# Performance work log

Hardware: AMD Instinct MI355X
Metric: run time of the kernel (lower is better)

Reference implementation:

```python
import jax, jax.numpy as jnp
import numpy as np

N, E, C, MID = 20000, 320000, 16, 32
EPS = 1e-8

# ---- real Clebsch-Gordan (Q_J) matrices for degree pairs up to l=1, real-SH m-order (-l..l) i.e. (y,z,x) for l=1 ----

def _q_matrices():
    Q0 = np.eye(3, dtype=np.float32)[:, :, None] / np.sqrt(3.0)          # 1x1 -> J=0
    eps = np.zeros((3, 3, 3), dtype=np.float32)
    for (a, b, c_) in [(0, 1, 2), (1, 2, 0), (2, 0, 1)]:
        eps[a, b, c_] = 1.0
        eps[a, c_, b] = -1.0
    Q1 = eps / np.sqrt(2.0)                                               # 1x1 -> J=1 (cross product)
    Q2 = np.zeros((3, 3, 5), dtype=np.float32)                            # 1x1 -> J=2 (sym traceless)
    s2 = 1.0 / np.sqrt(2.0); s6 = 1.0 / np.sqrt(6.0)
    Q2[2, 0, 0] = Q2[0, 2, 0] = s2          # ~xy
    Q2[0, 1, 1] = Q2[1, 0, 1] = s2          # ~yz
    Q2[0, 0, 2] = -s6; Q2[1, 1, 2] = 2 * s6; Q2[2, 2, 2] = -s6  # ~(2z2-x2-y2)
    Q2[1, 2, 3] = Q2[2, 1, 3] = s2          # ~xz
    Q2[2, 2, 4] = s2; Q2[0, 0, 4] = -s2     # ~(x2-y2)
    return Q0, Q1, Q2

_Q0, _Q1, _Q2 = _q_matrices()


def _basis(u):
    """u: [E,3] unit edge directions -> basis tensors per (d_in,d_out) pair."""
    x, y, z = u[:, 0], u[:, 1], u[:, 2]
    Ep = u.shape[0]
    Y0 = jnp.full((Ep,), 0.28209479177387814, u.dtype)
    Y1 = 0.4886025119029199 * jnp.stack([y, z, x], -1)                    # m=-1,0,1
    Y2 = jnp.stack([1.0925484305920792 * x * y,
                    1.0925484305920792 * y * z,
                    0.31539156525252005 * (3.0 * z * z - 1.0),
                    1.0925484305920792 * x * z,
                    0.5462742152960396 * (x * x - y * y)], -1)
    b00 = Y0.reshape(Ep, 1, 1, 1, 1, 1)
    b01 = Y1.reshape(Ep, 1, 3, 1, 1, 1)
    b10 = Y1.reshape(Ep, 1, 1, 1, 3, 1)
    K0 = Y0[:, None, None] * jnp.asarray(_Q0[:, :, 0])
    K1 = jnp.einsum('em,abm->eab', Y1, jnp.asarray(_Q1))
    K2 = jnp.einsum('em,abm->eab', Y2, jnp.asarray(_Q2))
    b11 = jnp.stack([K0, K1, K2], -1).reshape(Ep, 1, 3, 1, 3, 3)          # num_freq=3 (J=0,1,2)
    return b00, b01, b10, b11


def _bn(x, g, b):  # BatchNorm1d, training-mode stats over edges, eps=1e-5
    mu = x.mean(0)
    var = ((x - mu) ** 2).mean(0)
    return (x - mu) * jax.lax.rsqrt(var + 1e-5) * g + b


def _hidden(feat, W1, b1, g1, be1, W2, b2, g2, be2):
    h = jax.nn.relu(_bn(feat @ W1 + b1, g1, be1))
    return jax.nn.relu(_bn(h @ W2 + b2, g2, be2))


def _kernel(Rflat, basis, nco, do_dim, nci, di_dim, nf):
    # RadialFunc output view: [E, nc_out, 1, nc_in, 1, num_freq]; contract freq with basis
    R = Rflat.reshape(-1, nco, 1, nci, 1, nf)
    k = (R * basis).sum(-1)                        # [E,nco,do_dim,nci,di_dim]
    return k.reshape(-1, nco * do_dim, nci * di_dim)


def _norm_bias(x, bias):  # GNormBias: relu(|x| + b) * phase
    n = jnp.sqrt((x * x).sum(-1, keepdims=True) + 1e-12)
    phase = x / jnp.maximum(n, EPS)
    return jax.nn.relu(n[..., 0] + bias)[..., None] * phase


def _forward(src, dst, pos, c, v, w,
             rW1, rb1, rg1, rbe1, rW2, rb2, rg2, rbe2,
             w3_a00, b3_a00, w3_a01, b3_a01, w3_a10, b3_a10, w3_a11, b3_a11,
             w3_b01, b3_b01, w3_b11, b3_b11,
             selfA0, selfA1, selfB1, nbias0, nbias1):
    n_nodes = c.shape[0]
    n_edges = src.shape[0]
    rel = pos[dst] - pos[src]
    r = jnp.sqrt((rel * rel).sum(-1, keepdims=True))                      # [E,1]
    u = rel / jnp.maximum(r, EPS)
    b00, b01, b10, b11 = _basis(u)
    feat = jnp.concatenate([w, r], -1)                                    # [E, edge_dim+1]
    # all 6 radial-net hiddens at once: [6,E,MID]
    H = jax.vmap(_hidden, in_axes=(None, 0, 0, 0, 0, 0, 0, 0, 0))(
        feat, rW1, rb1, rg1, rbe1, rW2, rb2, rg2, rbe2)
    deg = jax.ops.segment_sum(jnp.ones((n_edges,), feat.dtype), dst, num_segments=n_nodes)
    inv = (1.0 / jnp.maximum(deg, 1.0))[:, None, None]
    mask = (deg > 0).astype(feat.dtype)[:, None, None]
    # ---- layer A: in {0:1,1:1} -> mid {0:C,1:C} ----
    k00 = _kernel(H[0] @ w3_a00 + b3_a00, b00, C, 1, 1, 1, 1)             # [E,C,1]
    k01 = _kernel(H[1] @ w3_a01 + b3_a01, b01, C, 3, 1, 1, 1)             # [E,3C,1]
    k10 = _kernel(H[2] @ w3_a10 + b3_a10, b10, C, 1, 1, 3, 1)             # [E,C,3]
    k11 = _kernel(H[3] @ w3_a11 + b3_a11, b11, C, 3, 1, 3, 3)             # [E,3C,3]
    s0 = c[src].reshape(n_edges, 1, 1)
    s1 = v[src].reshape(n_edges, 3, 1)
    m0 = (k00 @ s0 + k10 @ s1).reshape(n_edges, C, 1)
    m1 = (k01 @ s0 + k11 @ s1).reshape(n_edges, C, 3)
    h0 = jax.ops.segment_sum(m0, dst, num_segments=n_nodes) * inv \
         + jnp.einsum('oi,nid->nod', selfA0[0], c) * mask
    h1 = jax.ops.segment_sum(m1, dst, num_segments=n_nodes) * inv \
         + jnp.einsum('oi,nid->nod', selfA1[0], v) * mask
    # ---- GNormBias on mid fiber ----
    h0 = _norm_bias(h0, nbias0)
    h1 = _norm_bias(h1, nbias1)
    # ---- layer B: mid {0:C,1:C} -> out {1:2} ----
    kb01 = _kernel(H[4] @ w3_b01 + b3_b01, b01, 2, 3, C, 1, 1)            # [E,6,C]
    kb11 = _kernel(H[5] @ w3_b11 + b3_b11, b11, 2, 3, C, 3, 3)            # [E,6,3C]
    t0 = h0[src]                                                          # [E,C,1]
    t1 = h1[src].reshape(n_edges, C * 3, 1)
    mB = (kb01 @ t0 + kb11 @ t1).reshape(n_edges, 2, 3)
    out = jax.ops.segment_sum(mB, dst, num_segments=n_nodes) * inv \
          + jnp.einsum('oi,nid->nod', selfB1[0], h1) * mask
    return out                                                            # [N,2,3]


def setup_inputs() -> dict:
    key = jax.random.key(0)
    ks = jax.random.split(key, 40)
    def rn(i, shape, scale=1.0):
        return jax.random.normal(ks[i], shape, jnp.float32) * scale
    K = 6
    sc = 1.0 / np.sqrt(MID)
    d = {}
    d['src'] = jax.random.randint(ks[0], (E,), 0, N)
    d['dst'] = jax.random.randint(ks[1], (E,), 0, N)
    d['pos'] = rn(2, (N, 3))
    d['c'] = rn(3, (N, 1, 1))
    d['v'] = rn(4, (N, 1, 3))
    d['w'] = rn(5, (E, 1))
    d['rW1'] = rn(6, (K, 2, MID), 1.0 / np.sqrt(2.0))
    d['rb1'] = jnp.zeros((K, MID), jnp.float32)
    d['rg1'] = jnp.ones((K, MID), jnp.float32)
    d['rbe1'] = jnp.zeros((K, MID), jnp.float32)
    d['rW2'] = rn(7, (K, MID, MID), sc)
    d['rb2'] = jnp.zeros((K, MID), jnp.float32)
    d['rg2'] = jnp.ones((K, MID), jnp.float32)
    d['rbe2'] = jnp.zeros((K, MID), jnp.float32)
    d['w3_a00'] = rn(8, (MID, C), sc);      d['b3_a00'] = jnp.zeros((C,), jnp.float32)
    d['w3_a01'] = rn(9, (MID, C), sc);      d['b3_a01'] = jnp.zeros((C,), jnp.float32)
    d['w3_a10'] = rn(10, (MID, C), sc);     d['b3_a10'] = jnp.zeros((C,), jnp.float32)
    d['w3_a11'] = rn(11, (MID, 3 * C), sc); d['b3_a11'] = jnp.zeros((3 * C,), jnp.float32)
    d['w3_b01'] = rn(12, (MID, 2 * C), sc); d['b3_b01'] = jnp.zeros((2 * C,), jnp.float32)
    d['w3_b11'] = rn(13, (MID, 6 * C), sc); d['b3_b11'] = jnp.zeros((6 * C,), jnp.float32)
    d['selfA0'] = rn(14, (1, C, 1))
    d['selfA1'] = rn(15, (1, C, 1))
    d['selfB1'] = rn(16, (1, 2, C), 1.0 / np.sqrt(C))
    d['nbias0'] = rn(17, (C,))
    d['nbias1'] = rn(18, (C,))
    return d


def reference(src, dst, pos, c, v, w,
              rW1, rb1, rg1, rbe1, rW2, rb2, rg2, rbe2,
              w3_a00, b3_a00, w3_a01, b3_a01, w3_a10, b3_a10, w3_a11, b3_a11,
              w3_b01, b3_b01, w3_b11, b3_b11,
              selfA0, selfA1, selfB1, nbias0, nbias1):
    return _forward(src, dst, pos, c, v, w,
                    rW1, rb1, rg1, rbe1, rW2, rb2, rg2, rbe2,
                    w3_a00, b3_a00, w3_a01, b3_a01, w3_a10, b3_a10, w3_a11, b3_a11,
                    w3_b01, b3_b01, w3_b11, b3_b11,
                    selfA0, selfA1, selfB1, nbias0, nbias1)
```

## Files before the change

### kernel.cpp

```cpp
#include <hip/hip_runtime.h>

#define NN 20000
#define NE 320000
#define CDIM 16
#define MID 32
#define EPSF 1e-8f

#define SCHED_FENCE() __builtin_amdgcn_sched_barrier(0)

#define OFF_DEGI   848
#define ZERO_WORDS 20848
#define OFF_ROWPTR 20848
#define OFF_CURSOR 40864
#define OFF_EORDER 60864
#define OFF_SRCS   380864
#define OFF_WSRT   700864
#define OFF_FW1A   1020864
#define OFF_FW1B   1021056
#define OFF_FC1    1021248
#define OFF_BN2A   1021440
#define OFF_FC2    1021632
#define OFF_FW2T   1021824
#define OFF_ECS    1027968
#define OFF_H0N    2307968
#define OFF_H1N    2627968
#define OFF_MSGA0  3587968
#define OFF_MSGA1  8707968
#define OFF_MSGB   24067968

#define Y0C   0.28209479177387814f
#define Y1C   0.4886025119029199f
#define Y2C1  1.0925484305920792f
#define Y2C2  0.31539156525252005f
#define Y2C3  0.5462742152960396f
#define S2C   0.7071067811865476f
#define S6C   0.4082482904638631f
#define K0C   0.16286750396763996f

__device__ __forceinline__ void atomAddD(double* p, double v) {
  unsafeAtomicAdd(p, v);
}

__device__ __forceinline__ void mlpH_lds(
    const float* __restrict__ a1, const float* __restrict__ b1v,
    const float* __restrict__ c1, const float* __restrict__ c2,
    const float* __restrict__ W2T, float we, float r, float* H) {
  float h[MID];
#pragma unroll
  for (int j4 = 0; j4 < 8; ++j4) {
    float4 av = ((const float4*)a1)[j4];
    float4 bv = ((const float4*)b1v)[j4];
    float4 cv = ((const float4*)c1)[j4];
    h[4 * j4 + 0] = fmaxf(fmaf(we, av.x, fmaf(r, bv.x, cv.x)), 0.0f);
    h[4 * j4 + 1] = fmaxf(fmaf(we, av.y, fmaf(r, bv.y, cv.y)), 0.0f);
    h[4 * j4 + 2] = fmaxf(fmaf(we, av.z, fmaf(r, bv.z, cv.z)), 0.0f);
    h[4 * j4 + 3] = fmaxf(fmaf(we, av.w, fmaf(r, bv.w, cv.w)), 0.0f);
  }
  SCHED_FENCE();
#pragma unroll
  for (int jg = 0; jg < 8; ++jg) {
#pragma unroll
    for (int jq = 0; jq < 4; ++jq) {
      const int j = jg * 4 + jq;
      float acc = c2[j];
      const float4* wp = (const float4*)(W2T + j * MID);
#pragma unroll
      for (int i4 = 0; i4 < 8; ++i4) {
        float4 wv = wp[i4];
        acc = fmaf(h[4 * i4 + 0], wv.x, acc);
        acc = fmaf(h[4 * i4 + 1], wv.y, acc);
        acc = fmaf(h[4 * i4 + 2], wv.z, acc);
        acc = fmaf(h[4 * i4 + 3], wv.w, acc);
      }
      H[j] = fmaxf(acc, 0.0f);
    }
    SCHED_FENCE();
  }
}

__device__ __forceinline__ void mlpH2_lds(
    const float* __restrict__ a1, const float* __restrict__ b1v,
    const float* __restrict__ c1, const float* __restrict__ c2,
    const float* __restrict__ W2T,
    float weA, float rA, float weB, float rB,
    float* HA, float* HB) {
  float hA[MID], hB[MID];
#pragma unroll
  for (int j4 = 0; j4 < 8; ++j4) {
    float4 av = ((const float4*)a1)[j4];
    float4 bv = ((const float4*)b1v)[j4];
    float4 cv = ((const float4*)c1)[j4];
    hA[4 * j4 + 0] = fmaxf(fmaf(weA, av.x, fmaf(rA, bv.x, cv.x)), 0.0f);
    hB[4 * j4 + 0] = fmaxf(fmaf(weB, av.x, fmaf(rB, bv.x, cv.x)), 0.0f);
    hA[4 * j4 + 1] = fmaxf(fmaf(weA, av.y, fmaf(rA, bv.y, cv.y)), 0.0f);
    hB[4 * j4 + 1] = fmaxf(fmaf(weB, av.y, fmaf(rB, bv.y, cv.y)), 0.0f);
    hA[4 * j4 + 2] = fmaxf(fmaf(weA, av.z, fmaf(rA, bv.z, cv.z)), 0.0f);
    hB[4 * j4 + 2] = fmaxf(fmaf(weB, av.z, fmaf(rB, bv.z, cv.z)), 0.0f);
    hA[4 * j4 + 3] = fmaxf(fmaf(weA, av.w, fmaf(rA, bv.w, cv.w)), 0.0f);
    hB[4 * j4 + 3] = fmaxf(fmaf(weB, av.w, fmaf(rB, bv.w, cv.w)), 0.0f);
  }
  SCHED_FENCE();
#pragma unroll
  for (int jg = 0; jg < 8; ++jg) {
#pragma unroll
    for (int jq = 0; jq < 4; ++jq) {
      const int j = jg * 4 + jq;
      float c2v = c2[j];
      float accA = c2v, accB = c2v;
      const float4* wp = (const float4*)(W2T + j * MID);
#pragma unroll
      for (int i4 = 0; i4 < 8; ++i4) {
        float4 wv = wp[i4];
        accA = fmaf(hA[4 * i4 + 0], wv.x, accA);
        accB = fmaf(hB[4 * i4 + 0], wv.x, accB);
        accA = fmaf(hA[4 * i4 + 1], wv.y, accA);
        accB = fmaf(hB[4 * i4 + 1], wv.y, accB);
        accA = fmaf(hA[4 * i4 + 2], wv.z, accA);
        accB = fmaf(hB[4 * i4 + 2], wv.z, accB);
        accA = fmaf(hA[4 * i4 + 3], wv.w, accA);
        accB = fmaf(hB[4 * i4 + 3], wv.w, accB);
      }
      HA[j] = fmaxf(accA, 0.0f);
      HB[j] = fmaxf(accB, 0.0f);
    }
    SCHED_FENCE();
  }
}

__global__ __launch_bounds__(256) void k_hist(
    const int* __restrict__ dst, float* __restrict__ ws) {
  int e = blockIdx.x * blockDim.x + threadIdx.x;
  if (e >= NE) return;
  atomicAdd((int*)ws + OFF_DEGI + dst[e], 1);
}

__global__ void k_scan(float* __restrict__ ws) {
  __shared__ int buf[256];
  __shared__ int carry;
  const int* degi = (const int*)ws + OFF_DEGI;
  int* rowptr = (int*)ws + OFF_ROWPTR;
  int* cursor = (int*)ws + OFF_CURSOR;
  int tid = threadIdx.x;
  if (tid == 0) carry = 0;
  __syncthreads();
  for (int base = 0; base < NN; base += 256) {
    int v = (base + tid < NN) ? degi[base + tid] : 0;
    buf[tid] = v;
    __syncthreads();
    for (int off = 1; off < 256; off <<= 1) {
      int t = buf[tid];
      int add = (tid >= off) ? buf[tid - off] : 0;
      __syncthreads();
      buf[tid] = t + add;
      __syncthreads();
    }
    int excl = buf[tid] - v;
    if (base + tid < NN) {
      rowptr[base + tid] = carry + excl;
      cursor[base + tid] = carry + excl;
    }
    __syncthreads();
    if (tid == 255) carry += buf[255];
    __syncthreads();
  }
  if (tid == 0) rowptr[NN] = carry;
}

__global__ __launch_bounds__(256) void k_scatter(
    const int* __restrict__ dst, float* __restrict__ ws) {
  int e = blockIdx.x * blockDim.x + threadIdx.x;
  if (e >= NE) return;
  int* cursor = (int*)ws + OFF_CURSOR;
  int* eorder = (int*)ws + OFF_EORDER;
  int d = dst[e];
  int p = atomicAdd(cursor + d, 1);
  eorder[p] = e;
}

__global__ __launch_bounds__(256) void k_geo(
    const int* __restrict__ src, const int* __restrict__ dst,
    const float* __restrict__ pos, const float* __restrict__ w,
    float* __restrict__ ws) {
  __shared__ double sred[20];
  double lw = 0, lr = 0, lww = 0, lrr = 0, lwr = 0;
  const int* eorder = (const int*)ws + OFF_EORDER;
  int* srcs = (int*)ws + OFF_SRCS;
  float* wsrt = ws + OFF_WSRT;
  float4* ecs = (float4*)(ws + OFF_ECS);
  for (int t = blockIdx.x * blockDim.x + threadIdx.x; t < NE;
       t += gridDim.x * blockDim.x) {
    int e = eorder[t];
    int s = src[e], d = dst[e];
    float dx = pos[3 * d + 0] - pos[3 * s + 0];
    float dy = pos[3 * d + 1] - pos[3 * s + 1];
    float dz = pos[3 * d + 2] - pos[3 * s + 2];
    float r = sqrtf(dx * dx + dy * dy + dz * dz);
    float ri = 1.0f / fmaxf(r, EPSF);
    ecs[t] = make_float4(r, dx * ri, dy * ri, dz * ri);
    float we = w[e];
    wsrt[t] = we;
    srcs[t] = s;
    double wd = (double)we, rd = (double)r;
    lw += wd; lr += rd; lww += wd * wd; lrr += rd * rd; lwr += wd * rd;
  }
#pragma unroll
  for (int d = 32; d >= 1; d >>= 1) {
    lw += __shfl_xor(lw, d);
    lr += __shfl_xor(lr, d);
    lww += __shfl_xor(lww, d);
    lrr += __shfl_xor(lrr, d);
    lwr += __shfl_xor(lwr, d);
  }
  int wid = threadIdx.x >> 6;
  if ((threadIdx.x & 63) == 0) {
    sred[0 * 4 + wid] = lw;
    sred[1 * 4 + wid] = lr;
    sred[2 * 4 + wid] = lww;
    sred[3 * 4 + wid] = lrr;
    sred[4 * 4 + wid] = lwr;
  }
  __syncthreads();
  if (threadIdx.x < 5) {
    double v = sred[threadIdx.x * 4 + 0] + sred[threadIdx.x * 4 + 1]
             + sred[threadIdx.x * 4 + 2] + sred[threadIdx.x * 4 + 3];
    atomAddD((double*)ws + threadIdx.x * 8, v);
  }
}

__global__ void k_fin1(const float* __restrict__ rW1, const float* __restrict__ rb1,
                       const float* __restrict__ rg1, const float* __restrict__ rbe1,
                       float* __restrict__ ws) {
  int t = threadIdx.x;
  int k = t >> 5, j = t & 31;
  const double* s1 = (const double*)ws;
  double Sw = s1[0], Sr = s1[8], Sww = s1[16], Srr = s1[24], Swr = s1[32];
  const double inv = 1.0 / (double)NE;
  double W0 = (double)rW1[k * 64 + j], W1 = (double)rW1[k * 64 + 32 + j];
  double b = (double)rb1[k * 32 + j];
  double mlin = (Sw * W0 + Sr * W1) * inv;
  double mu = mlin + b;
  double ex2 = (Sww * W0 * W0 + Srr * W1 * W1 + 2.0 * Swr * W0 * W1) * inv
             + 2.0 * b * mlin + b * b;
  double var = ex2 - mu * mu;
  double a = (double)rg1[k * 32 + j] / sqrt(var + 1e-5);
  ws[OFF_FW1A + t] = (float)(W0 * a);
  ws[OFF_FW1B + t] = (float)(W1 * a);
  ws[OFF_FC1 + t] = (float)((double)rbe1[k * 32 + j] - mlin * a);
}

__global__ __launch_bounds__(256) void k_stats2(
    const float* __restrict__ rW2, const float* __restrict__ rb2,
    float* __restrict__ ws) {
  const int k = blockIdx.y;
  const int j0 = blockIdx.z * 16;
  __shared__ __align__(16) float sW1a[32], sW1b[32], sc1[32];
  __shared__ __align__(16) float sW2c[512];
  __shared__ float sb2[16];
  __shared__ float sredf[2][16][4];
  int tid = threadIdx.x;
  if (tid < 32) {
    sW1a[tid] = ws[OFF_FW1A + k * 32 + tid];
    sW1b[tid] = ws[OFF_FW1B + k * 32 + tid];
    sc1[tid] = ws[OFF_FC1 + k * 32 + tid];
  }
  if (tid < 16) sb2[tid] = rb2[k * 32 + j0 + tid];
  for (int t = tid; t < 512; t += 256) {
    int jj = t >> 5, i = t & 31;
    sW2c[t] = rW2[k * 1024 + i * 32 + j0 + jj];
  }
  __syncthreads();
  const float4* ecs = (const float4*)(ws + OFF_ECS);
  const float* wsrt = ws + OFF_WSRT;
  float lsum[16], lsq[16];
#pragma unroll
  for (int jj = 0; jj < 16; ++jj) { lsum[jj] = 0.0f; lsq[jj] = 0.0f; }
  const int NP = NE / 2;
  for (int p = blockIdx.x * blockDim.x + tid; p < NP;
       p += gridDim.x * blockDim.x) {
    int e0 = 2 * p;
    float r0 = ecs[e0].x, r1 = ecs[e0 + 1].x;
    float w0 = wsrt[e0], w1 = wsrt[e0 + 1];
    float h0[MID], h1[MID];
#pragma unroll
    for (int j4 = 0; j4 < 8; ++j4) {
      float4 av = ((const float4*)sW1a)[j4];
      float4 bv = ((const float4*)sW1b)[j4];
      float4 cv = ((const float4*)sc1)[j4];
      h0[4 * j4 + 0] = fmaxf(fmaf(w0, av.x, fmaf(r0, bv.x, cv.x)), 0.0f);
      h1[4 * j4 + 0] = fmaxf(fmaf(w1, av.x, fmaf(r1, bv.x, cv.x)), 0.0f);
      h0[4 * j4 + 1] = fmaxf(fmaf(w0, av.y, fmaf(r0, bv.y, cv.y)), 0.0f);
      h1[4 * j4 + 1] = fmaxf(fmaf(w1, av.y, fmaf(r1, bv.y, cv.y)), 0.0f);
      h0[4 * j4 + 2] = fmaxf(fmaf(w0, av.z, fmaf(r0, bv.z, cv.z)), 0.0f);
      h1[4 * j4 + 2] = fmaxf(fmaf(w1, av.z, fmaf(r1, bv.z, cv.z)), 0.0f);
      h0[4 * j4 + 3] = fmaxf(fmaf(w0, av.w, fmaf(r0, bv.w, cv.w)), 0.0f);
      h1[4 * j4 + 3] = fmaxf(fmaf(w1, av.w, fmaf(r1, bv.w, cv.w)), 0.0f);
    }
    SCHED_FENCE();
#pragma unroll
    for (int jg = 0; jg < 4; ++jg) {
#pragma unroll
      for (int jq = 0; jq < 4; ++jq) {
        const int jj = jg * 4 + jq;
        float aE0 = sb2[jj], aE1 = sb2[jj];
        const float4* wp = (const float4*)(sW2c + jj * 32);
#pragma unroll
        for (int i4 = 0; i4 < 8; ++i4) {
          float4 wv = wp[i4];
          aE0 = fmaf(h0[4 * i4 + 0], wv.x, aE0);
          aE1 = fmaf(h1[4 * i4 + 0], wv.x, aE1);
          aE0 = fmaf(h0[4 * i4 + 1], wv.y, aE0);
          aE1 = fmaf(h1[4 * i4 + 1], wv.y, aE1);
          aE0 = fmaf(h0[4 * i4 + 2], wv.z, aE0);
          aE1 = fmaf(h1[4 * i4 + 2], wv.z, aE1);
          aE0 = fmaf(h0[4 * i4 + 3], wv.w, aE0);
          aE1 = fmaf(h1[4 * i4 + 3], wv.w, aE1);
        }
        lsum[jj] += aE0 + aE1;
        lsq[jj] = fmaf(aE0, aE0, fmaf(aE1, aE1, lsq[jj]));
      }
      SCHED_FENCE();
    }
  }
  int wid = tid >> 6;
#pragma unroll
  for (int jj = 0; jj < 16; ++jj) {
    float v1 = lsum[jj], v2 = lsq[jj];
#pragma unroll
    for (int d = 32; d >= 1; d >>= 1) {
      v1 += __shfl_xor(v1, d);
      v2 += __shfl_xor(v2, d);
    }
    if ((tid & 63) == 0) {
      sredf[0][jj][wid] = v1;
      sredf[1][jj][wid] = v2;
    }
  }
  __syncthreads();
  if (tid < 32) {
    int jj = tid & 15, which = tid >> 4;
    float v = sredf[which][jj][0] + sredf[which][jj][1]
            + sredf[which][jj][2] + sredf[which][jj][3];
    double* s2 = (double*)(ws + 80);
    atomAddD(s2 + k * 64 + which * 32 + j0 + jj, (double)v);
  }
}

__global__ void k_fin2(const float* __restrict__ rb2,
                       const float* __restrict__ rg2, const float* __restrict__ rbe2,
                       float* __restrict__ ws) {
  int t = threadIdx.x;
  int k = t >> 5, j = t & 31;
  const double* s2 = (const double*)(ws + 80);
  const double inv = 1.0 / (double)NE;
  double mu = s2[k * 64 + j] * inv;
  double ex2 = s2[k * 64 + 32 + j] * inv;
  double var = ex2 - mu * mu;
  double a = (double)rg2[t] / sqrt(var + 1e-5);
  ws[OFF_BN2A + t] = (float)a;
  ws[OFF_FC2 + t] = (float)((double)rbe2[t] + ((double)rb2[t] - mu) * a);
}

__global__ __launch_bounds__(256) void k_fold2(const float* __restrict__ rW2,
                                               float* __restrict__ ws) {
  int idx = blockIdx.x * blockDim.x + threadIdx.x;
  if (idx >= 6144) return;
  int k = idx >> 10, rem = idx & 1023;
  int j = rem >> 5, i = rem & 31;
  ws[OFF_FW2T + idx] = rW2[k * 1024 + i * 32 + j] * ws[OFF_BN2A + k * 32 + j];
}

__global__ __launch_bounds__(256) void k_passA0(
    const float* __restrict__ cI, const float* __restrict__ vI,
    const float* __restrict__ w00, const float* __restrict__ b00,
    const float* __restrict__ w10, const float* __restrict__ b10,
    float* __restrict__ ws) {
  __shared__ __align__(16) float sW1a[64], sW1b[64], sc1[64], sc2[64];
  __shared__ __align__(16) float sW2T[2048];
  __shared__ __align__(16) float sP00[512], sP10[512];
  __shared__ float sB00[16], sB10[16];
  int tid = threadIdx.x;
  if (tid < 32) {
    sW1a[tid] = ws[OFF_FW1A + tid];       sW1a[32 + tid] = ws[OFF_FW1A + 64 + tid];
    sW1b[tid] = ws[OFF_FW1B + tid];       sW1b[32 + tid] = ws[OFF_FW1B + 64 + tid];
    sc1[tid]  = ws[OFF_FC1 + tid];        sc1[32 + tid]  = ws[OFF_FC1 + 64 + tid];
    sc2[tid]  = ws[OFF_FC2 + tid];        sc2[32 + tid]  = ws[OFF_FC2 + 64 + tid];
  }
  for (int t = tid; t < 2048; t += 256) {
    sW2T[t] = ws[OFF_FW2T + ((t < 1024) ? t : (1024 + t))];
  }
  for (int t = tid; t < 512; t += 256) {
    int i = t >> 4, co = t & 15;
    sP00[co * 32 + i] = w00[t];
    sP10[co * 32 + i] = w10[t];
  }
  if (tid < 16) { sB00[tid] = b00[tid]; sB10[tid] = b10[tid]; }
  __syncthreads();

  const int* srcs = (const int*)ws + OFF_SRCS;
  const float* wsrt = ws + OFF_WSRT;
  const float4* ecs = (const float4*)(ws + OFF_ECS);
  int t = blockIdx.x * blockDim.x + tid;
  if (t >= NE) return;
  int s = srcs[t];
  float4 E = ecs[t];
  float we = wsrt[t];
  float cs = cI[s];
  float v0 = vI[3 * s + 0], v1 = vI[3 * s + 1], v2 = vI[3 * s + 2];
  float dY1v = Y1C * (E.z * v0 + E.w * v1 + E.y * v2);

  float H[MID], m0[CDIM];
  mlpH_lds(sW1a, sW1b, sc1, sc2, sW2T, we, E.x, H);
  float f0 = Y0C * cs;
#pragma unroll
  for (int cg = 0; cg < 4; ++cg) {
#pragma unroll
    for (int cq = 0; cq < 4; ++cq) {
      const int co = cg * 4 + cq;
      float a = sB00[co];
      const float4* wp = (const float4*)(sP00 + co * 32);
#pragma unroll
      for (int i4 = 0; i4 < 8; ++i4) {
        float4 wv = wp[i4];
        a = fmaf(H[4 * i4 + 0], wv.x, a);
        a = fmaf(H[4 * i4 + 1], wv.y, a);
        a = fmaf(H[4 * i4 + 2], wv.z, a);
        a = fmaf(H[4 * i4 + 3], wv.w, a);
      }
      m0[co] = a * f0;
    }
    SCHED_FENCE();
  }
  mlpH_lds(sW1a + 32, sW1b + 32, sc1 + 32, sc2 + 32, sW2T + 1024, we, E.x, H);
#pragma unroll
  for (int cg = 0; cg < 4; ++cg) {
#pragma unroll
    for (int cq = 0; cq < 4; ++cq) {
      const int co = cg * 4 + cq;
      float a = sB10[co];
      const float4* wp = (const float4*)(sP10 + co * 32);
#pragma unroll
      for (int i4 = 0; i4 < 8; ++i4) {
        float4 wv = wp[i4];
        a = fmaf(H[4 * i4 + 0], wv.x, a);
        a = fmaf(H[4 * i4 + 1], wv.y, a);
        a = fmaf(H[4 * i4 + 2], wv.z, a);
        a = fmaf(H[4 * i4 + 3], wv.w, a);
      }
      m0[co] = fmaf(a, dY1v, m0[co]);
    }
    SCHED_FENCE();
  }
  float4* mp = (float4*)(ws + OFF_MSGA0) + t * 4;
#pragma unroll
  for (int q = 0; q < 4; ++q)
    mp[q] = make_float4(m0[4 * q], m0[4 * q + 1], m0[4 * q + 2], m0[4 * q + 3]);
}

__global__ __launch_bounds__(256) void k_passA1(
    const float* __restrict__ cI, const float* __restrict__ vI,
    const float* __restrict__ w01, const float* __restrict__ b01,
    const float* __restrict__ w11, const float* __restrict__ b11,
    float* __restrict__ ws) {
  __shared__ __align__(16) float sW1a[64], sW1b[64], sc1[64], sc2[64];
  __shared__ __align__(16) float sW2T[2048];
  __shared__ __align__(16) float sP01[512], sP11[1536];
  __shared__ float sB01[16], sB11[48];
  int tid = threadIdx.x;
  if (tid < 32) {
    sW1a[tid] = ws[OFF_FW1A + 32 + tid];  sW1a[32 + tid] = ws[OFF_FW1A + 96 + tid];
    sW1b[tid] = ws[OFF_FW1B + 32 + tid];  sW1b[32 + tid] = ws[OFF_FW1B + 96 + tid];
    sc1[tid]  = ws[OFF_FC1 + 32 + tid];   sc1[32 + tid]  = ws[OFF_FC1 + 96 + tid];
    sc2[tid]  = ws[OFF_FC2 + 32 + tid];   sc2[32 + tid]  = ws[OFF_FC2 + 96 + tid];
  }
  for (int t = tid; t < 1024; t += 256) {
    sW2T[t] = ws[OFF_FW2T + 1024 + t];
    sW2T[1024 + t] = ws[OFF_FW2T + 3072 + t];
  }
  for (int t = tid; t < 512; t += 256) {
    int i = t >> 4, co = t & 15;
    sP01[co * 32 + i] = w01[t];
  }
  for (int t = tid; t < 1536; t += 256) {
    int i = t / 48, c = t - i * 48;
    sP11[c * 32 + i] = w11[t];
  }
  if (tid < 16) sB01[tid] = b01[tid];
  if (tid < 48) sB11[tid] = b11[tid];
  __syncthreads();

  const int* srcs = (const int*)ws + OFF_SRCS;
  const float* wsrt = ws + OFF_WSRT;
  const float4* ecs = (const float4*)(ws + OFF_ECS);
  int t = blockIdx.x * blockDim.x + tid;
  if (t >= NE) return;
  int s = srcs[t];
  float4 E = ecs[t];
  float we = wsrt[t];
  float cs = cI[s];

  float H[MID];
  float ra[16];
  mlpH_lds(sW1a, sW1b, sc1, sc2, sW2T, we, E.x, H);
#pragma unroll
  for (int cg = 0; cg < 4; ++cg) {
#pragma unroll
    for (int cq = 0; cq < 4; ++cq) {
      const int co = cg * 4 + cq;
      float a = sB01[co];
      const float4* wp = (const float4*)(sP01 + co * 32);
#pragma unroll
      for (int i4 = 0; i4 < 8; ++i4) {
        float4 wv = wp[i4];
        a = fmaf(H[4 * i4 + 0], wv.x, a);
        a = fmaf(H[4 * i4 + 1], wv.y, a);
        a = fmaf(H[4 * i4 + 2], wv.z, a);
        a = fmaf(H[4 * i4 + 3], wv.w, a);
      }
      ra[co] = a;
    }
    SCHED_FENCE();
  }
  mlpH_lds(sW1a + 32, sW1b + 32, sc1 + 32, sc2 + 32, sW2T + 1024, we, E.x, H);
  float y10 = Y1C * E.z, y11 = Y1C * E.w, y12 = Y1C * E.y;
  float KV[3][3];
  {
    float ux = E.y, uy = E.z, uz = E.w;
    float y20 = Y2C1 * ux * uy, y21 = Y2C1 * uy * uz;
    float y22 = Y2C2 * (3.0f * uz * uz - 1.0f);
    float y23 = Y2C1 * ux * uz, y24 = Y2C3 * (ux * ux - uy * uy);
    float S00 = -S6C * y22 - S2C * y24;
    float S11 = 2.0f * S6C * y22;
    float S22 = -S6C * y22 + S2C * y24;
    float S01 = S2C * y21, S02 = S2C * y20, S12 = S2C * y23;
    float v0 = vI[3 * s + 0], v1 = vI[3 * s + 1], v2 = vI[3 * s + 2];
    KV[0][0] = K0C * v0; KV[0][1] = K0C * v1; KV[0][2] = K0C * v2;
    KV[1][0] = S2C * (y12 * v1 - y11 * v2);
    KV[1][1] = S2C * (y10 * v2 - y12 * v0);
    KV[1][2] = S2C * (y11 * v0 - y10 * v1);
    KV[2][0] = S00 * v0 + S01 * v1 + S02 * v2;
    KV[2][1] = S01 * v0 + S11 * v1 + S12 * v2;
    KV[2][2] = S02 * v0 + S12 * v1 + S22 * v2;
  }
  float cy0 = cs * y10, cy1 = cs * y11, cy2 = cs * y12;
#pragma unroll 1
  for (int g = 0; g < 4; ++g) {
    float a[12];
#pragma unroll
    for (int q = 0; q < 4; ++q) {
      int co = g * 4 + q;
      float R0 = sB11[co * 3 + 0], R1 = sB11[co * 3 + 1], R2 = sB11[co * 3 + 2];
      const float4* p0 = (const float4*)(sP11 + (co * 3 + 0) * 32);
      const float4* p1 = (const float4*)(sP11 + (co * 3 + 1) * 32);
      const float4* p2 = (const float4*)(sP11 + (co * 3 + 2) * 32);
#pragma unroll
      for (int i4 = 0; i4 < 8; ++i4) {
        float4 w0v = p0[i4], w1v = p1[i4], w2v = p2[i4];
        float h0 = H[4 * i4 + 0], h1 = H[4 * i4 + 1];
        float h2 = H[4 * i4 + 2], h3 = H[4 * i4 + 3];
        R0 = fmaf(h0, w0v.x, R0); R1 = fmaf(h0, w1v.x, R1); R2 = fmaf(h0, w2v.x, R2);
        R0 = fmaf(h1, w0v.y, R0); R1 = fmaf(h1, w1v.y, R1); R2 = fmaf(h1, w2v.y, R2);
        R0 = fmaf(h2, w0v.z, R0); R1 = fmaf(h2, w1v.z, R1); R2 = fmaf(h2, w2v.z, R2);
        R0 = fmaf(h3, w0v.w, R0); R1 = fmaf(h3, w1v.w, R1); R2 = fmaf(h3, w2v.w, R2);
      }
      float r_ = ra[co];
      a[q * 3 + 0] = fmaf(r_, cy0, R0 * KV[0][0] + R1 * KV[1][0] + R2 * KV[2][0]);
      a[q * 3 + 1] = fmaf(r_, cy1, R0 * KV[0][1] + R1 * KV[1][1] + R2 * KV[2][1]);
      a[q * 3 + 2] = fmaf(r_, cy2, R0 * KV[0][2] + R1 * KV[1][2] + R2 * KV[2][2]);
    }
    float4* mp = (float4*)(ws + OFF_MSGA1 + g * (NE * 12)) + t * 3;
    mp[0] = make_float4(a[0], a[1], a[2], a[3]);
    mp[1] = make_float4(a[4], a[5], a[6], a[7]);
    mp[2] = make_float4(a[8], a[9], a[10], a[11]);
    SCHED_FENCE();
  }
}

__global__ __launch_bounds__(256) void k_nodeA(
    const float* __restrict__ cI, const float* __restrict__ vI,
    const float* __restrict__ selfA0, const float* __restrict__ selfA1,
    const float* __restrict__ nbias0, const float* __restrict__ nbias1,
    float* __restrict__ ws) {
  int idx = blockIdx.x * blockDim.x + threadIdx.x;
  if (idx >= NN * CDIM) return;
  int n = idx >> 4, co = idx & 15;
  const int* rowptr = (const int*)ws + OFF_ROWPTR;
  int r0 = rowptr[n], r1 = rowptr[n + 1];
  const float* mA0 = ws + OFF_MSGA0;
  const float* mA1 = ws + OFF_MSGA1 + (co >> 2) * (NE * 12) + (co & 3) * 3;
  float x0 = 0.0f, xa = 0.0f, xb = 0.0f, xc = 0.0f;
  for (int row = r0; row < r1; ++row) {
    x0 += mA0[row * 16 + co];
    xa += mA1[row * 12 + 0];
    xb += mA1[row * 12 + 1];
    xc += mA1[row * 12 + 2];
  }
  float dg = (float)(r1 - r0);
  float iv = 1.0f / fmaxf(dg, 1.0f);
  float mk = dg > 0.0f ? 1.0f : 0.0f;
  x0 = x0 * iv + selfA0[co] * cI[n] * mk;
  float n0 = sqrtf(x0 * x0 + 1e-12f);
  ws[OFF_H0N + idx] = fmaxf(n0 + nbias0[co], 0.0f) * (x0 / fmaxf(n0, EPSF));
  xa = xa * iv + selfA1[co] * vI[3 * n + 0] * mk;
  xb = xb * iv + selfA1[co] * vI[3 * n + 1] * mk;
  xc = xc * iv + selfA1[co] * vI[3 * n + 2] * mk;
  float nv = sqrtf(xa * xa + xb * xb + xc * xc + 1e-12f);
  float sc = fmaxf(nv + nbias1[co], 0.0f) / fmaxf(nv, EPSF);
  ws[OFF_H1N + idx * 3 + 0] = xa * sc;
  ws[OFF_H1N + idx * 3 + 1] = xb * sc;
  ws[OFF_H1N + idx * 3 + 2] = xc * sc;
}

__global__ __launch_bounds__(256) void k_passB(
    const float* __restrict__ wb01, const float* __restrict__ bb01,
    const float* __restrict__ wb11, const float* __restrict__ bb11,
    float* __restrict__ ws) {
  __shared__ __align__(16) float sW1a[64], sW1b[64], sc1[64], sc2[64];
  __shared__ __align__(16) float sW2T[2048];
  __shared__ __align__(16) float sPB01[1024];
  __shared__ __align__(16) float sPB11[3072];
  __shared__ float sBB01[32];
  __shared__ float sBB11[96];
  int tid = threadIdx.x;
  if (tid < 64) {
    sW1a[tid] = ws[OFF_FW1A + 128 + tid];
    sW1b[tid] = ws[OFF_FW1B + 128 + tid];
    sc1[tid] = ws[OFF_FC1 + 128 + tid];
    sc2[tid] = ws[OFF_FC2 + 128 + tid];
  }
  for (int t = tid; t < 2048; t += 256) sW2T[t] = ws[OFF_FW2T + 4096 + t];
  for (int t = tid; t < 1024; t += 256) {
    int i = t >> 5, c = t & 31;
    int o = c >> 4, ci = c & 15;
    sPB01[(ci * 2 + o) * 32 + i] = wb01[t];
  }
  for (int t = tid; t < 3072; t += 256) {
    int i = t / 96, c = t - i * 96;
    int o = c / 48, rem = c - o * 48;
    int ci = rem / 3, f = rem - ci * 3;
    sPB11[(ci * 6 + o * 3 + f) * 32 + i] = wb11[t];
  }
  if (tid < 32) {
    int o = tid >> 4, ci = tid & 15;
    sBB01[ci * 2 + o] = bb01[tid];
  }
  if (tid < 96) {
    int o = tid / 48, rem = tid - o * 48;
    int ci = rem / 3, f = rem - ci * 3;
    sBB11[ci * 6 + o * 3 + f] = bb11[tid];
  }
  __syncthreads();

  const int* srcs = (const int*)ws + OFF_SRCS;
  const float* wsrt = ws + OFF_WSRT;
  const float4* ecs = (const float4*)(ws + OFF_ECS);
  const int NP = NE / 2;
  int p = blockIdx.x * blockDim.x + tid;
  if (p >= NP) return;
  {
    int tA = 2 * p, tB = 2 * p + 1;
    int sA = srcs[tA], sB_ = srcs[tB];
    float4 EA = ecs[tA], EB = ecs[tB];
    float weA = wsrt[tA], weB = wsrt[tB];

    float HA[MID], HB[MID];
    mlpH2_lds(sW1a, sW1b, sc1, sc2, sW2T, weA, EA.x, weB, EB.x, HA, HB);
    const float* h0pA = ws + OFF_H0N + sA * CDIM;
    const float* h0pB = ws + OFF_H0N + sB_ * CDIM;
    float A0A = 0.0f, A1A = 0.0f, A0B = 0.0f, A1B = 0.0f;
#pragma unroll 1
    for (int ci = 0; ci < CDIM; ++ci) {
      float bA = h0pA[ci], bB = h0pB[ci];
      float R0A = sBB01[ci * 2 + 0], R1A = sBB01[ci * 2 + 1];
      float R0B = R0A, R1B = R1A;
      const float4* p0 = (const float4*)(sPB01 + (ci * 2 + 0) * 32);
      const float4* p1 = (const float4*)(sPB01 + (ci * 2 + 1) * 32);
#pragma unroll
      for (int i4 = 0; i4 < 8; ++i4) {
        float4 w0v = p0[i4], w1v = p1[i4];
        float hA0 = HA[4 * i4 + 0], hB0 = HB[4 * i4 + 0];
        float hA1 = HA[4 * i4 + 1], hB1 = HB[4 * i4 + 1];
        float hA2 = HA[4 * i4 + 2], hB2 = HB[4 * i4 + 2];
        float hA3 = HA[4 * i4 + 3], hB3 = HB[4 * i4 + 3];
        R0A = fmaf(hA0, w0v.x, R0A); R0B = fmaf(hB0, w0v.x, R0B);
        R1A = fmaf(hA0, w1v.x, R1A); R1B = fmaf(hB0, w1v.x, R1B);
        R0A = fmaf(hA1, w0v.y, R0A); R0B = fmaf(hB1, w0v.y, R0B);
        R1A = fmaf(hA1, w1v.y, R1A); R1B = fmaf(hB1, w1v.y, R1B);
        R0A = fmaf(hA2, w0v.z, R0A); R0B = fmaf(hB2, w0v.z, R0B);
        R1A = fmaf(hA2, w1v.z, R1A); R1B = fmaf(hB2, w1v.z, R1B);
        R0A = fmaf(hA3, w0v.w, R0A); R0B = fmaf(hB3, w0v.w, R0B);
        R1A = fmaf(hA3, w1v.w, R1A); R1B = fmaf(hB3, w1v.w, R1B);
      }
      A0A = fmaf(R0A, bA, A0A); A1A = fmaf(R1A, bA, A1A);
      A0B = fmaf(R0B, bB, A0B); A1B = fmaf(R1B, bB, A1B);
      SCHED_FENCE();
    }
    mlpH2_lds(sW1a + 32, sW1b + 32, sc1 + 32, sc2 + 32, sW2T + 1024,
              weA, EA.x, weB, EB.x, HA, HB);
    const float* h1pA = ws + OFF_H1N + sA * CDIM * 3;
    const float* h1pB = ws + OFF_H1N + sB_ * CDIM * 3;
    float GA[6][3], GB[6][3];
#pragma unroll
    for (int of = 0; of < 6; ++of) {
      GA[of][0] = 0.0f; GA[of][1] = 0.0f; GA[of][2] = 0.0f;
      GB[of][0] = 0.0f; GB[of][1] = 0.0f; GB[of][2] = 0.0f;
    }
#pragma unroll 1
    for (int ci = 0; ci < CDIM; ++ci) {
      float bA0 = h1pA[ci * 3 + 0], bA1 = h1pA[ci * 3 + 1], bA2 = h1pA[ci * 3 + 2];
      float bB0 = h1pB[ci * 3 + 0], bB1 = h1pB[ci * 3 + 1], bB2 = h1pB[ci * 3 + 2];
#pragma unroll
      for (int of = 0; of < 6; ++of) {
        float RA = sBB11[ci * 6 + of];
        float RB = RA;
        const float4* wp = (const float4*)(sPB11 + (ci * 6 + of) * 32);
#pragma unroll
        for (int i4 = 0; i4 < 8; ++i4) {
          float4 wv = wp[i4];
          RA = fmaf(HA[4 * i4 + 0], wv.x, RA);
          RB = fmaf(HB[4 * i4 + 0], wv.x, RB);
          RA = fmaf(HA[4 * i4 + 1], wv.y, RA);
          RB = fmaf(HB[4 * i4 + 1], wv.y, RB);
          RA = fmaf(HA[4 * i4 + 2], wv.z, RA);
          RB = fmaf(HB[4 * i4 + 2], wv.z, RB);
          RA = fmaf(HA[4 * i4 + 3], wv.w, RA);
          RB = fmaf(HB[4 * i4 + 3], wv.w, RB);
        }
        GA[of][0] = fmaf(RA, bA0, GA[of][0]);
        GA[of][1] = fmaf(RA, bA1, GA[of][1]);
        GA[of][2] = fmaf(RA, bA2, GA[of][2]);
        GB[of][0] = fmaf(RB, bB0, GB[of][0]);
        GB[of][1] = fmaf(RB, bB1, GB[of][1]);
        GB[of][2] = fmaf(RB, bB2, GB[of][2]);
      }
      SCHED_FENCE();
    }
    {
      float ux = EA.y, uy = EA.z, uz = EA.w;
      float y10 = Y1C * uy, y11 = Y1C * uz, y12 = Y1C * ux;
      float y20 = Y2C1 * ux * uy, y21 = Y2C1 * uy * uz;
      float y22 = Y2C2 * (3.0f * uz * uz - 1.0f);
      float y23 = Y2C1 * ux * uz, y24 = Y2C3 * (ux * ux - uy * uy);
      float S00 = -S6C * y22 - S2C * y24;
      float S11 = 2.0f * S6C * y22;
      float S22 = -S6C * y22 + S2C * y24;
      float S01 = S2C * y21, S02 = S2C * y20, S12 = S2C * y23;
      float4* mp = (float4*)(ws + OFF_MSGB) + tA * 2;
#pragma unroll
      for (int o = 0; o < 2; ++o) {
        float Ao = (o == 0) ? A0A : A1A;
        float m0 = Ao * y10 + K0C * GA[o * 3 + 0][0]
                 + S2C * (y12 * GA[o * 3 + 1][1] - y11 * GA[o * 3 + 1][2])
                 + S00 * GA[o * 3 + 2][0] + S01 * GA[o * 3 + 2][1] + S02 * GA[o * 3 + 2][2];
        float m1 = Ao * y11 + K0C * GA[o * 3 + 0][1]
                 + S2C * (y10 * GA[o * 3 + 1][2] - y12 * GA[o * 3 + 1][0])
                 + S01 * GA[o * 3 + 2][0] + S11 * GA[o * 3 + 2][1] + S12 * GA[o * 3 + 2][2];
        float m2 = Ao * y12 + K0C * GA[o * 3 + 0][2]
                 + S2C * (y11 * GA[o * 3 + 1][0] - y10 * GA[o * 3 + 1][1])
                 + S02 * GA[o * 3 + 2][0] + S12 * GA[o * 3 + 2][1] + S22 * GA[o * 3 + 2][2];
        mp[o] = make_float4(m0, m1, m2, 0.0f);
      }
    }
    {
      float ux = EB.y, uy = EB.z, uz = EB.w;
      float y10 = Y1C * uy, y11 = Y1C * uz, y12 = Y1C * ux;
      float y20 = Y2C1 * ux * uy, y21 = Y2C1 * uy * uz;
      float y22 = Y2C2 * (3.0f * uz * uz - 1.0f);
      float y23 = Y2C1 * ux * uz, y24 = Y2C3 * (ux * ux - uy * uy);
      float S00 = -S6C * y22 - S2C * y24;
      float S11 = 2.0f * S6C * y22;
      float S22 = -S6C * y22 + S2C * y24;
      float S01 = S2C * y21, S02 = S2C * y20, S12 = S2C * y23;
      float4* mp = (float4*)(ws + OFF_MSGB) + tB * 2;
#pragma unroll
      for (int o = 0; o < 2; ++o) {
        float Ao = (o == 0) ? A0B : A1B;
        float m0 = Ao * y10 + K0C * GB[o * 3 + 0][0]
                 + S2C * (y12 * GB[o * 3 + 1][1] - y11 * GB[o * 3 + 1][2])
                 + S00 * GB[o * 3 + 2][0] + S01 * GB[o * 3 + 2][1] + S02 * GB[o * 3 + 2][2];
        float m1 = Ao * y11 + K0C * GB[o * 3 + 0][1]
                 + S2C * (y10 * GB[o * 3 + 1][2] - y12 * GB[o * 3 + 1][0])
                 + S01 * GB[o * 3 + 2][0] + S11 * GB[o * 3 + 2][1] + S12 * GB[o * 3 + 2][2];
        float m2 = Ao * y12 + K0C * GB[o * 3 + 0][2]
                 + S2C * (y11 * GB[o * 3 + 1][0] - y10 * GB[o * 3 + 1][1])
                 + S02 * GB[o * 3 + 2][0] + S12 * GB[o * 3 + 2][1] + S22 * GB[o * 3 + 2][2];
        mp[o] = make_float4(m0, m1, m2, 0.0f);
      }
    }
  }
}

__global__ __launch_bounds__(256) void k_nodeB(
    const float* __restrict__ selfB1, float* __restrict__ out,
    const float* __restrict__ ws) {
  int idx = blockIdx.x * blockDim.x + threadIdx.x;
  if (idx >= NN * 6) return;
  int n = idx / 6;
  int q = idx - n * 6;
  int o = q / 3, a = q - o * 3;
  const int* rowptr = (const int*)ws + OFF_ROWPTR;
  int r0 = rowptr[n], r1 = rowptr[n + 1];
  const float* msgB = ws + OFF_MSGB;
  int col = o * 4 + a;
  float sum = 0.0f;
  for (int row = r0; row < r1; ++row) sum += msgB[row * 8 + col];
  float dg = (float)(r1 - r0);
  float iv = 1.0f / fmaxf(dg, 1.0f);
  float mk = dg > 0.0f ? 1.0f : 0.0f;
  const float* h1p = ws + OFF_H1N + n * CDIM * 3;
  float self = 0.0f;
#pragma unroll
  for (int ci = 0; ci < CDIM; ++ci)
    self = fmaf(selfB1[o * CDIM + ci], h1p[ci * 3 + a], self);
  out[idx] = sum * iv + self * mk;
}

extern "C" void kernel_launch(void* const* d_in, const int* in_sizes, int n_in,
                              void* d_out, int out_size, void* d_ws, size_t ws_size,
                              hipStream_t stream) {
  (void)in_sizes; (void)n_in; (void)out_size; (void)ws_size;
  const int* src = (const int*)d_in[0];
  const int* dst = (const int*)d_in[1];
  const float* pos = (const float*)d_in[2];
  const float* cI = (const float*)d_in[3];
  const float* vI = (const float*)d_in[4];
  const float* w = (const float*)d_in[5];
  const float* rW1 = (const float*)d_in[6];
  const float* rb1 = (const float*)d_in[7];
  const float* rg1 = (const float*)d_in[8];
  const float* rbe1 = (const float*)d_in[9];
  const float* rW2 = (const float*)d_in[10];
  const float* rb2 = (const float*)d_in[11];
  const float* rg2 = (const float*)d_in[12];
  const float* rbe2 = (const float*)d_in[13];
  const float* w3_a00 = (const float*)d_in[14];
  const float* b3_a00 = (const float*)d_in[15];
  const float* w3_a01 = (const float*)d_in[16];
  const float* b3_a01 = (const float*)d_in[17];
  const float* w3_a10 = (const float*)d_in[18];
  const float* b3_a10 = (const float*)d_in[19];
  const float* w3_a11 = (const float*)d_in[20];
  const float* b3_a11 = (const float*)d_in[21];
  const float* w3_b01 = (const float*)d_in[22];
  const float* b3_b01 = (const float*)d_in[23];
  const float* w3_b11 = (const float*)d_in[24];
  const float* b3_b11 = (const float*)d_in[25];
  const float* selfA0 = (const float*)d_in[26];
  const float* selfA1 = (const float*)d_in[27];
  const float* selfB1 = (const float*)d_in[28];
  const float* nbias0 = (const float*)d_in[29];
  const float* nbias1 = (const float*)d_in[30];
  float* ws = (float*)d_ws;
  float* out = (float*)d_out;

  hipMemsetAsync(d_ws, 0, (size_t)ZERO_WORDS * 4, stream);

  k_hist<<<1250, 256, 0, stream>>>(dst, ws);
  k_scan<<<1, 256, 0, stream>>>(ws);
  k_scatter<<<1250, 256, 0, stream>>>(dst, ws);
  k_geo<<<1250, 256, 0, stream>>>(src, dst, pos, w, ws);
  k_fin1<<<1, 192, 0, stream>>>(rW1, rb1, rg1, rbe1, ws);
  k_stats2<<<dim3(256, 6, 2), 256, 0, stream>>>(rW2, rb2, ws);
  k_fin2<<<1, 192, 0, stream>>>(rb2, rg2, rbe2, ws);
  k_fold2<<<24, 256, 0, stream>>>(rW2, ws);
  k_passA0<<<1250, 256, 0, stream>>>(cI, vI, w3_a00, b3_a00, w3_a10, b3_a10, ws);
  k_passA1<<<1250, 256, 0, stream>>>(cI, vI, w3_a01, b3_a01, w3_a11, b3_a11, ws);
  k_nodeA<<<1250, 256, 0, stream>>>(cI, vI, selfA0, selfA1, nbias0, nbias1, ws);
  k_passB<<<625, 256, 0, stream>>>(w3_b01, b3_b01, w3_b11, b3_b11, ws);
  k_nodeB<<<469, 256, 0, stream>>>(selfB1, out, ws);
}
```

Baseline: 540.2 us.

## Replace single-block serial prefix scan with three-phase multi-block scan

The degree prefix scan ran in one 256-thread block looping over all 20000 nodes in 79 serial chunks, each with a barrier-heavy scan. It is now split into a per-block local scan over 79 blocks, a small scan of the block totals, and a pass that adds the offsets back. This turns a long serial single-CU step into parallel work, at the cost of two extra kernel launches. Block totals are parked temporarily in the eorder buffer before the scatter kernel overwrites it, and the final rowptr entry is set to the known edge count instead of being computed.

```diff
diff --git a/kernel.cpp b/kernel.cpp
--- a/kernel.cpp
+++ b/kernel.cpp
@@ -5,6 +5,7 @@
 #define CDIM 16
 #define MID 32
 #define EPSF 1e-8f
+#define NBLK 79
 
 #define SCHED_FENCE() __builtin_amdgcn_sched_barrier(0)
 
@@ -134,36 +135,56 @@
   atomicAdd((int*)ws + OFF_DEGI + dst[e], 1);
 }
 
-__global__ void k_scan(float* __restrict__ ws) {
+__global__ __launch_bounds__(256) void k_scan1(float* __restrict__ ws) {
   __shared__ int buf[256];
-  __shared__ int carry;
   const int* degi = (const int*)ws + OFF_DEGI;
   int* rowptr = (int*)ws + OFF_ROWPTR;
+  int* aux = (int*)ws + OFF_EORDER;
+  int tid = threadIdx.x;
+  int i = blockIdx.x * 256 + tid;
+  int v = (i < NN) ? degi[i] : 0;
+  buf[tid] = v;
+  __syncthreads();
+  for (int off = 1; off < 256; off <<= 1) {
+    int t = buf[tid];
+    int add = (tid >= off) ? buf[tid - off] : 0;
+    __syncthreads();
+    buf[tid] = t + add;
+    __syncthreads();
+  }
+  if (i < NN) rowptr[i] = buf[tid] - v;
+  if (tid == 255) aux[blockIdx.x] = buf[255];
+}
+
+__global__ void k_scan2(float* __restrict__ ws) {
+  __shared__ int s[128];
+  int* aux = (int*)ws + OFF_EORDER;
+  int tid = threadIdx.x;
+  int v = (tid < NBLK) ? aux[tid] : 0;
+  s[tid] = v;
+  __syncthreads();
+  for (int off = 1; off < 128; off <<= 1) {
+    int t = s[tid];
+    int add = (tid >= off) ? s[tid - off] : 0;
+    __syncthreads();
+    s[tid] = t + add;
+    __syncthreads();
+  }
+  if (tid < NBLK) aux[tid] = s[tid] - v;
+}
+
+__global__ __launch_bounds__(256) void k_scan3(float* __restrict__ ws) {
+  int* rowptr = (int*)ws + OFF_ROWPTR;
   int* cursor = (int*)ws + OFF_CURSOR;
+  const int* aux = (const int*)ws + OFF_EORDER;
   int tid = threadIdx.x;
-  if (tid == 0) carry = 0;
-  __syncthreads();
-  for (int base = 0; base < NN; base += 256) {
-    int v = (base + tid < NN) ? degi[base + tid] : 0;
-    buf[tid] = v;
-    __syncthreads();
-    for (int off = 1; off < 256; off <<= 1) {
-      int t = buf[tid];
-      int add = (tid >= off) ? buf[tid - off] : 0;
-      __syncthreads();
-      buf[tid] = t + add;
-      __syncthreads();
-    }
-    int excl = buf[tid] - v;
-    if (base + tid < NN) {
-      rowptr[base + tid] = carry + excl;
-      cursor[base + tid] = carry + excl;
-    }
-    __syncthreads();
-    if (tid == 255) carry += buf[255];
-    __syncthreads();
-  }
-  if (tid == 0) rowptr[NN] = carry;
+  int i = blockIdx.x * 256 + tid;
+  if (i < NN) {
+    int r = rowptr[i] + aux[blockIdx.x];
+    rowptr[i] = r;
+    cursor[i] = r;
+  }
+  if (i == 0) rowptr[NN] = NE;
 }
 
 __global__ __launch_bounds__(256) void k_scatter(
@@ -855,7 +876,9 @@
   hipMemsetAsync(d_ws, 0, (size_t)ZERO_WORDS * 4, stream);
 
   k_hist<<<1250, 256, 0, stream>>>(dst, ws);
-  k_scan<<<1, 256, 0, stream>>>(ws);
+  k_scan1<<<NBLK, 256, 0, stream>>>(ws);
+  k_scan2<<<1, 128, 0, stream>>>(ws);
+  k_scan3<<<NBLK, 256, 0, stream>>>(ws);
   k_scatter<<<1250, 256, 0, stream>>>(dst, ws);
   k_geo<<<1250, 256, 0, stream>>>(src, dst, pos, w, ws);
   k_fin1<<<1, 192, 0, stream>>>(rW1, rb1, rg1, rbe1, ws);
```

After: 468.1 us (median of 2 runs). -13.3%, faster.
